# Optimization experiments

Hardware: AMD Instinct MI355X
Metric: run time of the kernel (lower is better)

The kernel has to match this reference:

```python
import jax, jax.numpy as jnp
import numpy as np

H, R, B = 8192, 4, 64


def glorot(key, shape):
    return jax.random.uniform(key, shape, minval=-1.0, maxval=1.0) * jnp.sqrt(2.0 / sum(shape))


def setup_inputs() -> dict:
    key = jax.random.key(0)
    k1, k2, k3, k4, kh, kx = jax.random.split(key, 6)
    return {
        "h": jax.random.normal(kh, (B, H), dtype=jnp.float32),
        "x": jax.random.normal(kx, (B, H), dtype=jnp.float32),
        "a_diag": glorot(k1, (H,)).astype(jnp.float32),
        "p_vec": glorot(k2, (H, R)).astype(jnp.float32),
        "q_vec": glorot(k3, (H, R)).astype(jnp.float32),
        "b_mat": glorot(k4, (H, H)).astype(jnp.float32),
    }


def reference(h, x, a_diag, p_vec, q_vec, b_mat):
    # Faithful to the source: explicitly materialize the dense DPLR matrix
    # a_dplr = diag(a_diag) + p q^T  (H x H), then a_dplr @ h + b_mat.T @ x.
    a_dplr = jnp.diag(a_diag) + p_vec @ q_vec.T  # (H, H)
    # Batched over leading dim: (a_dplr @ h_i) == h @ a_dplr.T ; (b_mat.T @ x_i) == x @ b_mat
    return h @ a_dplr.T + x @ b_mat  # (B, H)
```

## Files before the change

kernel.cpp:

```cpp
#include <hip/hip_runtime.h>
#include <hip/hip_bf16.h>


#define HDIM 8192
#define BDIM 64
#define RDIM 4
#define KSPLIT 16
#define KSLAB 512
#define NKTILE (KSLAB / 32)

typedef short short8 __attribute__((ext_vector_type(8)));
typedef float f32x4 __attribute__((ext_vector_type(4)));
typedef float f32x16 __attribute__((ext_vector_type(16)));

__device__ __forceinline__ unsigned f2bf(float f) {
  unsigned u = __float_as_uint(f);
  unsigned r = u + 0x7fffu + ((u >> 16) & 1u);
  return r >> 16;
}

__device__ __forceinline__ float bf2f(unsigned short u) {
  return __uint_as_float(((unsigned)u) << 16);
}

__global__ __launch_bounds__(256)
void prep_hq_kernel(const float* __restrict__ x,
                    const float* __restrict__ h,
                    const float* __restrict__ q,
                    unsigned short* __restrict__ xb,
                    float* __restrict__ hq) {
  const int b = blockIdx.x, t = threadIdx.x;
  {
    const float* xrow = x + (size_t)b * HDIM;
    unsigned short* xo = xb + (size_t)b * HDIM;
#pragma unroll
    for (int i = 0; i < 4; ++i) {
      const int base = (t * 4 + i) * 8;
      f32x4 v0 = *(const f32x4*)(xrow + base);
      f32x4 v1 = *(const f32x4*)(xrow + base + 4);
      union { unsigned short u[8]; short8 s; } o;
#pragma unroll
      for (int e = 0; e < 4; ++e) {
        o.u[e] = (unsigned short)f2bf(v0[e]);
        o.u[4 + e] = (unsigned short)f2bf(v1[e]);
      }
      *(short8*)(xo + base) = o.s;
    }
  }
  const float* hrow = h + (size_t)b * HDIM;
  f32x4 s = {0.f, 0.f, 0.f, 0.f};
  for (int k = t; k < HDIM; k += 256) {
    float hv = hrow[k];
    f32x4 qv = *(const f32x4*)(q + (size_t)k * RDIM);
    s += hv * qv;
  }
  __shared__ f32x4 red[256];
  red[t] = s;
  __syncthreads();
  for (int off = 128; off > 0; off >>= 1) {
    if (t < off) red[t] += red[t + off];
    __syncthreads();
  }
  if (t == 0) *(f32x4*)(hq + (size_t)b * RDIM) = red[0];
}

__global__ __launch_bounds__(512, 2)
void dplr_main(const float* __restrict__ bmat,
               const unsigned short* __restrict__ xb,
               unsigned short* __restrict__ part) {
  __shared__ __align__(16) unsigned short xs[BDIM * KSLAB];

  const int t    = threadIdx.x;
  const int lane = t & 63;
  const int w    = t >> 6;
  const int c32  = lane & 31;
  const int kh   = lane >> 5;

  const int jg = blockIdx.x & 15;
  const int ks = blockIdx.x >> 4;
  const int k0 = ks * KSLAB;

  {
    const int row = t >> 3;
    const int kq0 = (t & 7) * 8;
    const unsigned short* src = xb + (size_t)row * HDIM + k0 + kq0 * 8;
#pragma unroll
    for (int i = 0; i < 8; ++i) {
      const int g  = row * (KSLAB / 8) + kq0 + i;
      const int gs = g ^ (row & 7);
      *(short8*)&xs[gs * 8] = *(const short8*)(src + i * 8);
    }
  }
  __syncthreads();

  const int j0 = jg * 512 + w * 64;
  const float* b0 = bmat + (size_t)k0 * HDIM + j0 + lane;

  f32x16 acc[2][2];
#pragma unroll
  for (int mt = 0; mt < 2; ++mt)
#pragma unroll
    for (int nt = 0; nt < 2; ++nt)
#pragma unroll
      for (int r = 0; r < 16; ++r) acc[mt][nt][r] = 0.f;

  float LA[32], LB[32];

  auto issue = [&](int tile, float* buf) {
#pragma unroll
    for (int i = 0; i < 32; ++i)
      buf[i] = b0[(size_t)(tile * 32 + i) * HDIM];
  };

  auto conv_mfma = [&](int tile, const float* buf) {
#pragma unroll
    for (int s = 0; s < 2; ++s) {
      unsigned wv[8];
#pragma unroll
      for (int i = 0; i < 8; ++i)
        wv[i] = f2bf(buf[s * 16 + 2 * i]) | (f2bf(buf[s * 16 + 2 * i + 1]) << 16);
#pragma unroll
      for (int j = 0; j < 4; ++j)
        asm volatile("v_permlane32_swap_b32 %0, %1"
                     : "+v"(wv[j]), "+v"(wv[4 + j]));
      union { unsigned u[4]; short8 v; } bf0, bf1;
#pragma unroll
      for (int j = 0; j < 4; ++j) { bf0.u[j] = wv[j]; bf1.u[j] = wv[4 + j]; }
#pragma unroll
      for (int mt = 0; mt < 2; ++mt) {
        const int row = mt * 32 + c32;
        const int gg  = row * (KSLAB / 8) + tile * 4 + s * 2 + kh;
        const int gs  = gg ^ (row & 7);
        short8 af = *(const short8*)&xs[gs * 8];
        acc[mt][0] = __builtin_amdgcn_mfma_f32_32x32x16_bf16(af, bf0.v, acc[mt][0], 0, 0, 0);
        acc[mt][1] = __builtin_amdgcn_mfma_f32_32x32x16_bf16(af, bf1.v, acc[mt][1], 0, 0, 0);
      }
    }
  };

  issue(0, LA);
  for (int tile = 0; tile < NKTILE; tile += 2) {
    issue(tile + 1, LB);
    conv_mfma(tile, LA);
    if (tile + 2 < NKTILE) issue(tile + 2, LA);
    conv_mfma(tile + 1, LB);
  }

  unsigned short* pb = part + (size_t)ks * BDIM * HDIM;
#pragma unroll
  for (int mt = 0; mt < 2; ++mt)
#pragma unroll
    for (int nt = 0; nt < 2; ++nt)
#pragma unroll
      for (int reg = 0; reg < 16; ++reg) {
        const int row = mt * 32 + (reg & 3) + 8 * (reg >> 2) + 4 * kh;
        const int col = j0 + nt * 32 + c32;
        pb[(size_t)row * HDIM + col] = (unsigned short)f2bf(acc[mt][nt][reg]);
      }
}

__global__ __launch_bounds__(256)
void combine_kernel(const unsigned short* __restrict__ part,
                    const float* __restrict__ h,
                    const float* __restrict__ adiag,
                    const float* __restrict__ pvec,
                    const float* __restrict__ hq,
                    float* __restrict__ out) {
  const int tid  = blockIdx.x * 256 + threadIdx.x;
  const int base = tid * 8;
  const int row  = base >> 13;
  const int j    = base & 8191;

  float s[8];
#pragma unroll
  for (int e = 0; e < 8; ++e) s[e] = 0.f;
  const unsigned short* pp = part + (size_t)row * HDIM + j;
#pragma unroll
  for (int ks = 0; ks < KSPLIT; ++ks) {
    union { unsigned short u[8]; short8 v; } pv;
    pv.v = *(const short8*)(pp + (size_t)ks * BDIM * HDIM);
#pragma unroll
    for (int e = 0; e < 8; ++e) s[e] += bf2f(pv.u[e]);
  }
  const f32x4 hv0 = *(const f32x4*)(h + (size_t)row * HDIM + j);
  const f32x4 hv1 = *(const f32x4*)(h + (size_t)row * HDIM + j + 4);
  const f32x4 a0  = *(const f32x4*)(adiag + j);
  const f32x4 a1  = *(const f32x4*)(adiag + j + 4);
  const f32x4 hqv = *(const f32x4*)(hq + (size_t)row * RDIM);

  float res[8];
#pragma unroll
  for (int e = 0; e < 4; ++e) {
    const f32x4 pv = *(const f32x4*)(pvec + (size_t)(j + e) * RDIM);
    res[e] = s[e] + hv0[e] * a0[e] +
             hqv[0] * pv[0] + hqv[1] * pv[1] + hqv[2] * pv[2] + hqv[3] * pv[3];
  }
#pragma unroll
  for (int e = 0; e < 4; ++e) {
    const f32x4 pv = *(const f32x4*)(pvec + (size_t)(j + 4 + e) * RDIM);
    res[4 + e] = s[4 + e] + hv1[e] * a1[e] +
                 hqv[0] * pv[0] + hqv[1] * pv[1] + hqv[2] * pv[2] + hqv[3] * pv[3];
  }
  f32x4 o0 = {res[0], res[1], res[2], res[3]};
  f32x4 o1 = {res[4], res[5], res[6], res[7]};
  *(f32x4*)(out + (size_t)row * HDIM + j) = o0;
  *(f32x4*)(out + (size_t)row * HDIM + j + 4) = o1;
}

extern "C" void kernel_launch(void* const* d_in, const int* in_sizes, int n_in,
                              void* d_out, int out_size, void* d_ws, size_t ws_size,
                              hipStream_t stream) {
  const float* h     = (const float*)d_in[0];
  const float* x     = (const float*)d_in[1];
  const float* adiag = (const float*)d_in[2];
  const float* pvec  = (const float*)d_in[3];
  const float* qvec  = (const float*)d_in[4];
  const float* bmat  = (const float*)d_in[5];
  float* out = (float*)d_out;

  unsigned short* xb = (unsigned short*)d_ws;
  float* hqbuf = (float*)((char*)d_ws + ((size_t)1 << 20));
  unsigned short* part = (unsigned short*)((char*)d_ws + ((size_t)2 << 20));

  prep_hq_kernel<<<BDIM, 256, 0, stream>>>(x, h, qvec, xb, hqbuf);
  dplr_main<<<KSPLIT * 16, 512, 0, stream>>>(bmat, xb, part);
  combine_kernel<<<(BDIM * HDIM / 8) / 256, 256, 0, stream>>>(part, h, adiag, pvec, hqbuf, out);
}
```

Before: 73.21 us.

## Fuse prep kernel into main GEMM: convert x in-block, compute hq in extra blocks

Removes the separate prep kernel launch. Each main block now reads fp32 x directly and converts its slab to bf16 while staging into LDS, and 64 extra blocks appended to the grid compute the h·q low-rank reduction. This drops one kernel launch and the round trip through the xb buffer. In exchange, x is converted redundantly by all 16 column-group blocks per k-slab, each reading twice the bytes of the old bf16 path.

```diff
diff --git a/kernel.cpp b/kernel.cpp
--- a/kernel.cpp
+++ b/kernel.cpp
@@ -23,54 +23,37 @@
   return __uint_as_float(((unsigned)u) << 16);
 }
 
-__global__ __launch_bounds__(256)
-void prep_hq_kernel(const float* __restrict__ x,
-                    const float* __restrict__ h,
-                    const float* __restrict__ q,
-                    unsigned short* __restrict__ xb,
-                    float* __restrict__ hq) {
-  const int b = blockIdx.x, t = threadIdx.x;
-  {
-    const float* xrow = x + (size_t)b * HDIM;
-    unsigned short* xo = xb + (size_t)b * HDIM;
-#pragma unroll
-    for (int i = 0; i < 4; ++i) {
-      const int base = (t * 4 + i) * 8;
-      f32x4 v0 = *(const f32x4*)(xrow + base);
-      f32x4 v1 = *(const f32x4*)(xrow + base + 4);
-      union { unsigned short u[8]; short8 s; } o;
-#pragma unroll
-      for (int e = 0; e < 4; ++e) {
-        o.u[e] = (unsigned short)f2bf(v0[e]);
-        o.u[4 + e] = (unsigned short)f2bf(v1[e]);
-      }
-      *(short8*)(xo + base) = o.s;
-    }
-  }
-  const float* hrow = h + (size_t)b * HDIM;
-  f32x4 s = {0.f, 0.f, 0.f, 0.f};
-  for (int k = t; k < HDIM; k += 256) {
-    float hv = hrow[k];
-    f32x4 qv = *(const f32x4*)(q + (size_t)k * RDIM);
-    s += hv * qv;
-  }
-  __shared__ f32x4 red[256];
-  red[t] = s;
-  __syncthreads();
-  for (int off = 128; off > 0; off >>= 1) {
-    if (t < off) red[t] += red[t + off];
-    __syncthreads();
-  }
-  if (t == 0) *(f32x4*)(hq + (size_t)b * RDIM) = red[0];
-}
-
 __global__ __launch_bounds__(512, 2)
 void dplr_main(const float* __restrict__ bmat,
-               const unsigned short* __restrict__ xb,
-               unsigned short* __restrict__ part) {
+               const float* __restrict__ x,
+               unsigned short* __restrict__ part,
+               const float* __restrict__ h,
+               const float* __restrict__ q,
+               float* __restrict__ hq) {
   __shared__ __align__(16) unsigned short xs[BDIM * KSLAB];
 
-  const int t    = threadIdx.x;
+  const int t = threadIdx.x;
+
+  if (blockIdx.x >= 256) {
+    const int b = blockIdx.x - 256;
+    const float* hrow = h + (size_t)b * HDIM;
+    f32x4 s = {0.f, 0.f, 0.f, 0.f};
+    for (int k = t; k < HDIM; k += 512) {
+      float hv = hrow[k];
+      f32x4 qv = *(const f32x4*)(q + (size_t)k * RDIM);
+      s += hv * qv;
+    }
+    f32x4* red = (f32x4*)xs;
+    red[t] = s;
+    __syncthreads();
+    for (int off = 256; off > 0; off >>= 1) {
+      if (t < off) red[t] += red[t + off];
+      __syncthreads();
+    }
+    if (t == 0) *(f32x4*)(hq + (size_t)b * RDIM) = red[0];
+    return;
+  }
+
   const int lane = t & 63;
   const int w    = t >> 6;
   const int c32  = lane & 31;
@@ -82,13 +65,20 @@
 
   {
     const int row = t >> 3;
-    const int kq0 = (t & 7) * 8;
-    const unsigned short* src = xb + (size_t)row * HDIM + k0 + kq0 * 8;
+    const float* src = x + (size_t)row * HDIM + k0 + (t & 7) * 64;
 #pragma unroll
     for (int i = 0; i < 8; ++i) {
-      const int g  = row * (KSLAB / 8) + kq0 + i;
+      f32x4 va = *(const f32x4*)(src + i * 8);
+      f32x4 vb = *(const f32x4*)(src + i * 8 + 4);
+      union { unsigned short u[8]; short8 s; } o;
+#pragma unroll
+      for (int e = 0; e < 4; ++e) {
+        o.u[e]     = (unsigned short)f2bf(va[e]);
+        o.u[4 + e] = (unsigned short)f2bf(vb[e]);
+      }
+      const int g  = row * (KSLAB / 8) + (t & 7) * 8 + i;
       const int gs = g ^ (row & 7);
-      *(short8*)&xs[gs * 8] = *(const short8*)(src + i * 8);
+      *(short8*)&xs[gs * 8] = o.s;
     }
   }
   __syncthreads();
@@ -218,11 +208,9 @@
   const float* bmat  = (const float*)d_in[5];
   float* out = (float*)d_out;
 
-  unsigned short* xb = (unsigned short*)d_ws;
-  float* hqbuf = (float*)((char*)d_ws + ((size_t)1 << 20));
-  unsigned short* part = (unsigned short*)((char*)d_ws + ((size_t)2 << 20));
-
-  prep_hq_kernel<<<BDIM, 256, 0, stream>>>(x, h, qvec, xb, hqbuf);
-  dplr_main<<<KSPLIT * 16, 512, 0, stream>>>(bmat, xb, part);
+  float* hqbuf = (float*)d_ws;
+  unsigned short* part = (unsigned short*)((char*)d_ws + ((size_t)1 << 20));
+
+  dplr_main<<<256 + BDIM, 512, 0, stream>>>(bmat, x, part, h, qvec, hqbuf);
   combine_kernel<<<(BDIM * HDIM / 8) / 256, 256, 0, stream>>>(part, h, adiag, pvec, hqbuf, out);
 }
```

Result: faster. 63.82 us (-12.8%).
